# Optimization experiments

Hardware: AMD Instinct MI355X
Metric: run time of the kernel (lower is better)

## Reference

```python
import jax, jax.numpy as jnp
import numpy as np

N = 100000
IN_CH = 128
HID = 16
HEADS = 8
OUT_CH = 16
E = 1600000
NEG_SLOPE = 0.2


def glorot(key, shape, fan_in, fan_out):
    lim = jnp.sqrt(6.0 / (fan_in + fan_out)).astype(jnp.float32)
    return jax.random.uniform(key, shape, jnp.float32, -lim, lim)


def setup_inputs() -> dict:
    key = jax.random.key(0)
    ks = jax.random.split(key, 10)
    x = jax.random.normal(ks[0], (N, IN_CH), jnp.float32)
    edge_index = jax.random.randint(ks[1], (2, E), 0, N, jnp.int32)
    # layer 1: GATConv(IN_CH, HID, heads=8), concat=True
    W1 = glorot(ks[2], (IN_CH, HEADS * HID), IN_CH, HEADS * HID)
    att_src1 = glorot(ks[3], (HEADS, HID), HID, 1)
    att_dst1 = glorot(ks[4], (HEADS, HID), HID, 1)
    b1 = jnp.zeros((HEADS * HID,), jnp.float32)
    # layer 2: GATConv(HID*8, OUT_CH, heads=1)
    W2 = glorot(ks[5], (HEADS * HID, OUT_CH), HEADS * HID, OUT_CH)
    att_src2 = glorot(ks[6], (1, OUT_CH), OUT_CH, 1)
    att_dst2 = glorot(ks[7], (1, OUT_CH), OUT_CH, 1)
    b2 = jnp.zeros((OUT_CH,), jnp.float32)
    return {"x": x, "edge_index": edge_index, "W1": W1, "att_src1": att_src1,
            "att_dst1": att_dst1, "b1": b1, "W2": W2, "att_src2": att_src2,
            "att_dst2": att_dst2, "b2": b2}


def gat_layer(x, src, tgt, W, a_src, a_dst, bias, heads, ch, n):
    # h: [N, H, C]
    h = (x @ W).reshape(n, heads, ch)
    alpha_s = jnp.sum(h * a_src[None], axis=-1)  # [N, H]
    alpha_d = jnp.sum(h * a_dst[None], axis=-1)  # [N, H]
    # per-edge attention logit (message flows src -> tgt)
    e = jax.nn.leaky_relu(alpha_s[src] + alpha_d[tgt], NEG_SLOPE)  # [E, H]
    # segment softmax over target node neighborhoods (stable)
    m = jax.ops.segment_max(e, tgt, num_segments=n)  # [N, H]
    e = jnp.exp(e - m[tgt])
    denom = jax.ops.segment_sum(e, tgt, num_segments=n)
    alpha = e / (denom[tgt] + 1e-16)  # [E, H]
    # weighted scatter-add of source features
    out = jax.ops.segment_sum(h[src] * alpha[:, :, None], tgt, num_segments=n)
    return out.reshape(n, heads * ch) + bias


def reference(x, edge_index, W1, att_src1, att_dst1, b1, W2, att_src2, att_dst2, b2):
    n = x.shape[0]
    loops = jnp.arange(n, dtype=edge_index.dtype)
    src = jnp.concatenate([edge_index[0], loops])
    tgt = jnp.concatenate([edge_index[1], loops])
    h = gat_layer(x, src, tgt, W1, att_src1, att_dst1, b1, HEADS, HID, n)
    h = jax.nn.elu(h)
    out = gat_layer(h, src, tgt, W2, att_src2, att_dst2, b2, 1, OUT_CH, n)
    return out
```

## Files before the change

kernel.cpp:

```cpp
#include <hip/hip_runtime.h>
#include <hip/hip_fp16.h>
#include <math.h>

#define IN_CH 128
#define HEADS 8
#define HID 16
#define OUT_CH 16
#define NEG 0.2f
#define NPB 256
#define MAXBUCK 400
#define AST 136

__device__ __forceinline__ float lrelu(float x){ return x > 0.f ? x : NEG * x; }
__device__ __forceinline__ float elu_fast(float x){ return x > 0.f ? x : __expf(x) - 1.f; }

typedef _Float16 half8 __attribute__((ext_vector_type(8)));
typedef float    f32x4 __attribute__((ext_vector_type(4)));

__global__ __launch_bounds__(256) void k_bhist(const int* __restrict__ tgt, int E, int nbuck, int epb,
                                               int* __restrict__ bcnt){
    __shared__ int hist[MAXBUCK];
    int tid = threadIdx.x;
    for (int i = tid; i < nbuck; i += 256) hist[i] = 0;
    __syncthreads();
    int start = blockIdx.x * epb, end = min(start + epb, E);
    for (int e = start + tid; e < end; e += 256) atomicAdd(&hist[tgt[e] >> 8], 1);
    __syncthreads();
    for (int i = tid; i < nbuck; i += 256) if (hist[i]) atomicAdd(&bcnt[i], hist[i]);
}

__global__ void k_bscan(const int* __restrict__ bcnt, int nbuck, int E,
                        int* __restrict__ boffs, int* __restrict__ bcur){
    __shared__ int s[512];
    int t = threadIdx.x;
    int v = (t < nbuck) ? bcnt[t] : 0;
    int orig = v;
    s[t] = v; __syncthreads();
    for (int off = 1; off < 512; off <<= 1){
        int u = (t >= off) ? s[t - off] : 0;
        __syncthreads();
        v += u; s[t] = v; __syncthreads();
    }
    if (t < nbuck){ boffs[t] = v - orig; bcur[t] = v - orig; }
    if (t == 0) boffs[nbuck] = E;
}

__global__ __launch_bounds__(256) void k_bscatter(const int* __restrict__ ei, int E, int nbuck, int epb,
                                                  int* __restrict__ bcur, int2* __restrict__ ebuck){
    __shared__ int hist[MAXBUCK];
    __shared__ int base[MAXBUCK];
    int tid = threadIdx.x;
    for (int i = tid; i < nbuck; i += 256) hist[i] = 0;
    __syncthreads();
    int start = blockIdx.x * epb, end = min(start + epb, E);
    for (int e = start + tid; e < end; e += 256) atomicAdd(&hist[ei[E + e] >> 8], 1);
    __syncthreads();
    for (int i = tid; i < nbuck; i += 256){
        base[i] = hist[i] ? atomicAdd(&bcur[i], hist[i]) : 0;
        hist[i] = 0;
    }
    __syncthreads();
    for (int e = start + tid; e < end; e += 256){
        int s = ei[e], t = ei[E + e];
        int b = t >> 8;
        int r = atomicAdd(&hist[b], 1);
        ebuck[base[b] + r] = make_int2(s, t);
    }
}

__global__ __launch_bounds__(256) void k_csr(const int2* __restrict__ ebuck, const int* __restrict__ boffs,
                                             int N, int E,
                                             int* __restrict__ offs, int* __restrict__ esrc){
    __shared__ int cnt[256];
    __shared__ int sscan[256];
    __shared__ int wcur[256];
    int b = blockIdx.x;
    int tid = threadIdx.x;
    int n0 = b * 256;
    int nn = min(256, N - n0);
    cnt[tid] = (tid < nn) ? 1 : 0;
    __syncthreads();
    int e0 = boffs[b], e1 = boffs[b + 1];
    for (int e = e0 + tid; e < e1; e += 256) atomicAdd(&cnt[ebuck[e].y & 255], 1);
    __syncthreads();
    int v = cnt[tid], orig = v;
    sscan[tid] = v; __syncthreads();
    for (int off = 1; off < 256; off <<= 1){
        int u = (tid >= off) ? sscan[tid - off] : 0;
        __syncthreads();
        v += u; sscan[tid] = v; __syncthreads();
    }
    int excl = v - orig;
    int gbase = e0 + n0;
    if (tid < nn){
        offs[n0 + tid] = gbase + excl;
        esrc[gbase + excl] = n0 + tid;
    }
    wcur[tid] = excl + 1;
    __syncthreads();
    for (int e = e0 + tid; e < e1; e += 256){
        int2 p = ebuck[e];
        int r = atomicAdd(&wcur[p.y & 255], 1);
        esrc[gbase + r] = p.x;
    }
    if (b == 0 && tid == 0) offs[N] = E + N;
}

__global__ __launch_bounds__(256) void k_gemm1(const float* __restrict__ x, const float* __restrict__ W1,
                                               __half* __restrict__ h1, int N, int NT){
    __shared__ _Float16 sB[128*AST];
    __shared__ _Float16 sA[2][64*AST];
    int tid = threadIdx.x;
    for (int i = tid; i < 128*128; i += 256){
        int k = i >> 7, c = i & 127;
        sB[c*AST + k] = (_Float16)W1[i];
    }
    int wave = tid >> 6, lane = tid & 63;
    int m = lane & 15, quad = lane >> 4;
    int rbase = wave * 16;

    float4 vr[8];
    int tile = blockIdx.x;
    #pragma unroll
    for (int i = 0; i < 8; ++i){
        int q = i*256 + tid;
        int r = q >> 5, seg = q & 31;
        int row = tile*64 + r;
        vr[i] = make_float4(0.f,0.f,0.f,0.f);
        if (tile < NT && row < N) vr[i] = *(const float4*)(x + (size_t)row*128 + seg*4);
    }
    int b = 0;
    for (; tile < NT; tile += gridDim.x){
        #pragma unroll
        for (int i = 0; i < 8; ++i){
            int q = i*256 + tid;
            int r = q >> 5, seg = q & 31;
            _Float16* dst = &sA[b][r*AST + seg*4];
            dst[0]=(_Float16)vr[i].x; dst[1]=(_Float16)vr[i].y;
            dst[2]=(_Float16)vr[i].z; dst[3]=(_Float16)vr[i].w;
        }
        __syncthreads();
        int tn = tile + gridDim.x;
        #pragma unroll
        for (int i = 0; i < 8; ++i){
            int q = i*256 + tid;
            int r = q >> 5, seg = q & 31;
            int row = tn*64 + r;
            vr[i] = make_float4(0.f,0.f,0.f,0.f);
            if (tn < NT && row < N) vr[i] = *(const float4*)(x + (size_t)row*128 + seg*4);
        }
        f32x4 acc[8] = {};
        #pragma unroll
        for (int kc = 0; kc < 4; ++kc){
            int kb = kc*32 + quad*8;
            half8 a = *(half8*)(&sA[b][(rbase + m)*AST + kb]);
            #pragma unroll
            for (int t = 0; t < 8; ++t){
                half8 bb = *(half8*)(&sB[(t*16 + m)*AST + kb]);
                acc[t] = __builtin_amdgcn_mfma_f32_16x16x32_f16(a, bb, acc[t], 0, 0, 0);
            }
        }
        int row0 = tile*64;
        #pragma unroll
        for (int t = 0; t < 8; ++t){
            #pragma unroll
            for (int j = 0; j < 4; ++j){
                int r = row0 + rbase + quad*4 + j;
                if (r < N) h1[(size_t)r*128 + t*16 + m] = __float2half(acc[t][j]);
            }
        }
        b ^= 1;
    }
}

struct H8 { __half2 v[8]; };

__global__ void k_alpha1(const __half2* __restrict__ h1h, const float* __restrict__ asrc, const float* __restrict__ adst,
                         float2* __restrict__ asw, float* __restrict__ ad1,
                         unsigned char* __restrict__ h1q, int N){
    int idx = blockIdx.x*blockDim.x + threadIdx.x;
    if (idx >= N*HEADS) return;
    int h = idx & 7;
    int n = idx >> 3;
    H8 blk = *(const H8*)(h1h + (size_t)n*64 + h*8);
    const float2* sp = (const float2*)(asrc + h*16);
    const float2* dp = (const float2*)(adst + h*16);
    float fv[16];
    float ss = 0.f, dd = 0.f;
    #pragma unroll
    for (int j = 0; j < 8; ++j){
        float2 v = __half22float2(blk.v[j]);
        fv[2*j] = v.x; fv[2*j+1] = v.y;
        float2 a = sp[j], b = dp[j];
        ss += v.x*a.x + v.y*a.y;
        dd += v.x*b.x + v.y*b.y;
    }
    float mx = 1e-12f;
    #pragma unroll
    for (int k = 0; k < 16; ++k) mx = fmaxf(mx, fabsf(fv[k]));
    float rs = 127.f / mx;
    unsigned int w[4];
    #pragma unroll
    for (int d = 0; d < 4; ++d){
        unsigned int b0 = (unsigned int)((int)rintf(fv[4*d+0]*rs) + 128);
        unsigned int b1 = (unsigned int)((int)rintf(fv[4*d+1]*rs) + 128);
        unsigned int b2 = (unsigned int)((int)rintf(fv[4*d+2]*rs) + 128);
        unsigned int b3 = (unsigned int)((int)rintf(fv[4*d+3]*rs) + 128);
        w[d] = b0 | (b1 << 8) | (b2 << 16) | (b3 << 24);
    }
    asw[idx] = make_float2(ss, mx * (1.f/127.f));
    ad1[idx] = dd;
    *(uint4*)(h1q + (size_t)idx*16) = make_uint4(w[0], w[1], w[2], w[3]);
}

__global__ __launch_bounds__(256) void k_agg1(const unsigned char* __restrict__ h1q, const float2* __restrict__ asw,
                                              const float* __restrict__ ad1,
                                              const int* __restrict__ offs, const int* __restrict__ esrc,
                                              const float* __restrict__ b1, __half2* __restrict__ hl2h,
                                              int nbase, int nend){
    int wv = threadIdx.x >> 6;
    int l  = threadIdx.x & 63;
    int nsub = l >> 5;
    int slot = (l >> 3) & 3;
    int c    = l & 7;
    int n = nbase + blockIdx.x*8 + wv*2 + nsub;
    bool alive = (n < nend);
    float adc = 0.f;
    int e0 = 0, deg = 0;
    if (alive){
        adc = ad1[n*8 + c];
        e0 = offs[n];
        deg = offs[n+1] - e0;
    }
    int degmax = max(deg, __shfl_xor(deg, 32));

    float acc[16] = {};
    float den = 0.f;
    float dq  = 0.f;
    for (int i = 0; i < degmax; i += 8){
        int j0 = i + slot, j1 = i + 4 + slot;
        bool v0 = j0 < deg, v1 = j1 < deg;
        int iA = e0 + (v0 ? j0 : 0);
        int iB = e0 + (v1 ? j1 : 0);
        int s0 = esrc[iA], s1 = esrc[iB];
        float2 aw0 = asw[s0*8 + c];
        float2 aw1 = asw[s1*8 + c];
        uint4 q0 = *(const uint4*)(h1q + (size_t)s0*128 + c*16);
        uint4 q1 = *(const uint4*)(h1q + (size_t)s1*128 + c*16);
        float w0 = v0 ? __expf(lrelu(aw0.x + adc)) : 0.f;
        float w1 = v1 ? __expf(lrelu(aw1.x + adc)) : 0.f;
        float wq0 = w0 * aw0.y;
        float wq1 = w1 * aw1.y;
        den += w0 + w1;
        dq  += wq0 + wq1;
        const unsigned int* u0 = (const unsigned int*)&q0;
        const unsigned int* u1 = (const unsigned int*)&q1;
        #pragma unroll
        for (int d = 0; d < 4; ++d){
            unsigned int a = u0[d], b = u1[d];
            acc[4*d+0] += wq0 * (float)(a & 255u);
            acc[4*d+1] += wq0 * (float)((a >> 8) & 255u);
            acc[4*d+2] += wq0 * (float)((a >> 16) & 255u);
            acc[4*d+3] += wq0 * (float)(a >> 24);
            acc[4*d+0] += wq1 * (float)(b & 255u);
            acc[4*d+1] += wq1 * (float)((b >> 8) & 255u);
            acc[4*d+2] += wq1 * (float)((b >> 16) & 255u);
            acc[4*d+3] += wq1 * (float)(b >> 24);
        }
    }
    den += __shfl_xor(den, 8);  den += __shfl_xor(den, 16);
    dq  += __shfl_xor(dq, 8);   dq  += __shfl_xor(dq, 16);
    #pragma unroll
    for (int k = 0; k < 16; ++k){
        acc[k] += __shfl_xor(acc[k], 8);
        acc[k] += __shfl_xor(acc[k], 16);
    }
    if (!alive) return;
    float rd = 1.f / (den + 1e-16f);
    float bias128 = 128.f * dq;
    float sel0, sel1, sel2, sel3;
    {
        float a0 = (slot & 1) ? acc[4]  : acc[0];
        float b0 = (slot & 1) ? acc[12] : acc[8];
        sel0 = (slot & 2) ? b0 : a0;
        float a1 = (slot & 1) ? acc[5]  : acc[1];
        float b1v = (slot & 1) ? acc[13] : acc[9];
        sel1 = (slot & 2) ? b1v : a1;
        float a2 = (slot & 1) ? acc[6]  : acc[2];
        float b2v = (slot & 1) ? acc[14] : acc[10];
        sel2 = (slot & 2) ? b2v : a2;
        float a3 = (slot & 1) ? acc[7]  : acc[3];
        float b3v = (slot & 1) ? acc[15] : acc[11];
        sel3 = (slot & 2) ? b3v : a3;
    }
    float4 b4 = *(const float4*)(b1 + c*16 + slot*4);
    float v0 = elu_fast((sel0 - bias128)*rd + b4.x);
    float v1 = elu_fast((sel1 - bias128)*rd + b4.y);
    float v2 = elu_fast((sel2 - bias128)*rd + b4.z);
    float v3 = elu_fast((sel3 - bias128)*rd + b4.w);
    __half2 q0h = __floats2half2_rn(v0, v1);
    __half2 q1h = __floats2half2_rn(v2, v3);
    float2 ov;
    *(__half2*)&ov.x = q0h; *(__half2*)&ov.y = q1h;
    *(float2*)(hl2h + (size_t)n*64 + c*8 + slot*2) = ov;
}

#define FMA4(acc, a, b) { acc.x += (a)*(b).x; acc.y += (a)*(b).y; acc.z += (a)*(b).z; acc.w += (a)*(b).w; }

__global__ __launch_bounds__(256) void k_gemm2(const __half2* __restrict__ hl2h, const float* __restrict__ W2,
                                               const float* __restrict__ asrc2, const float* __restrict__ adst2,
                                               __half2* __restrict__ h2h, float* __restrict__ as2, float* __restrict__ ad2,
                                               int N){
    __shared__ float sX[64*132];
    __shared__ float sW2[128*16];
    int tid = threadIdx.x;
    for (int i = tid; i < 128*16; i += 256) sW2[i] = W2[i];
    int row0 = blockIdx.x * 64;
    #pragma unroll
    for (int i = 0; i < 4; ++i){
        int q = i*256 + tid;
        int r = q >> 4, seg = q & 15;
        float4 raw = make_float4(0.f,0.f,0.f,0.f);
        if (row0 + r < N) raw = ((const float4*)(hl2h + (size_t)(row0+r)*64))[seg];
        const __half2* hp = (const __half2*)&raw;
        float* dst = &sX[r*132 + seg*8];
        #pragma unroll
        for (int j = 0; j < 4; ++j){
            float2 f = __half22float2(hp[j]);
            dst[2*j] = f.x; dst[2*j+1] = f.y;
        }
    }
    __syncthreads();
    int nd = tid >> 2;
    int cq = tid & 3, c0 = cq*4;
    int n = row0 + nd;
    float4 acc = make_float4(0.f,0.f,0.f,0.f);
    #pragma unroll 4
    for (int k4 = 0; k4 < 32; ++k4){
        float4 a  = *(const float4*)(&sX[nd*132 + k4*4]);
        float4 w0 = *(const float4*)(&sW2[(k4*4+0)*16 + c0]);
        float4 w1 = *(const float4*)(&sW2[(k4*4+1)*16 + c0]);
        float4 w2 = *(const float4*)(&sW2[(k4*4+2)*16 + c0]);
        float4 w3 = *(const float4*)(&sW2[(k4*4+3)*16 + c0]);
        FMA4(acc, a.x, w0); FMA4(acc, a.y, w1); FMA4(acc, a.z, w2); FMA4(acc, a.w, w3);
    }
    float ps = acc.x*asrc2[c0] + acc.y*asrc2[c0+1] + acc.z*asrc2[c0+2] + acc.w*asrc2[c0+3];
    float pd = acc.x*adst2[c0] + acc.y*adst2[c0+1] + acc.z*adst2[c0+2] + acc.w*adst2[c0+3];
    ps += __shfl_xor(ps, 1); ps += __shfl_xor(ps, 2);
    pd += __shfl_xor(pd, 1); pd += __shfl_xor(pd, 2);
    if (n < N){
        __half2 p0 = __floats2half2_rn(acc.x, acc.y);
        __half2 p1 = __floats2half2_rn(acc.z, acc.w);
        float2 ov;
        *(__half2*)&ov.x = p0; *(__half2*)&ov.y = p1;
        *(float2*)(h2h + (size_t)n*8 + cq*2) = ov;
        if (cq == 0){ as2[n] = ps; ad2[n] = pd; }
    }
}

__global__ __launch_bounds__(256) void k_agg2(const __half2* __restrict__ h2h, const float* __restrict__ as2v,
                                              const float* __restrict__ ad2v,
                                              const int* __restrict__ offs, const int* __restrict__ esrc,
                                              const float* __restrict__ b2, float* __restrict__ out, int N){
    int n = blockIdx.x*4 + (threadIdx.x >> 6);
    if (n >= N) return;
    int l = threadIdx.x & 63;
    int e0 = offs[n], e1 = offs[n+1];
    float ad = ad2v[n];
    int eo = l >> 3, c2 = l & 7;
    float ax = 0.f, ay = 0.f, den = 0.f;
    for (int e = e0 + eo; e < e1; e += 8){
        int s = esrc[e];
        float w = __expf(lrelu(as2v[s] + ad));
        den += w;
        float2 f = __half22float2(h2h[(size_t)s*8 + c2]);
        ax += w * f.x; ay += w * f.y;
    }
    ax += __shfl_xor(ax, 8);  ay += __shfl_xor(ay, 8);  den += __shfl_xor(den, 8);
    ax += __shfl_xor(ax, 16); ay += __shfl_xor(ay, 16); den += __shfl_xor(den, 16);
    ax += __shfl_xor(ax, 32); ay += __shfl_xor(ay, 32); den += __shfl_xor(den, 32);
    if (eo == 0){
        float rd = 1.f / (den + 1e-16f);
        float2 bb = *(const float2*)(b2 + c2*2);
        float2 o = make_float2(ax*rd + bb.x, ay*rd + bb.y);
        *(float2*)(out + (size_t)n*16 + c2*2) = o;
    }
}

extern "C" void kernel_launch(void* const* d_in, const int* in_sizes, int n_in,
                              void* d_out, int out_size, void* d_ws, size_t ws_size,
                              hipStream_t stream){
    const float* x     = (const float*)d_in[0];
    const int*   ei    = (const int*)  d_in[1];
    const float* W1    = (const float*)d_in[2];
    const float* asrc1 = (const float*)d_in[3];
    const float* adst1 = (const float*)d_in[4];
    const float* b1    = (const float*)d_in[5];
    const float* W2    = (const float*)d_in[6];
    const float* asrc2 = (const float*)d_in[7];
    const float* adst2 = (const float*)d_in[8];
    const float* b2    = (const float*)d_in[9];
    float* out = (float*)d_out;

    const int N = in_sizes[0] / IN_CH;
    const int E = in_sizes[1] / 2;
    const int ETOT = E + N;
    const int NBUCK = (N + NPB - 1) / NPB;

    char* p = (char*)d_ws;
    auto alloc = [&](size_t bytes) -> char* {
        char* r = p; p += (bytes + 255) & ~(size_t)255; return r;
    };
    __half2* h1h  = (__half2*)alloc((size_t)N * 64 * 4);
    __half2* hl2h = (__half2*)alloc((size_t)N * 64 * 4);
    unsigned char* h1q = (unsigned char*)alloc((size_t)N * 128);
    float2* asw  = (float2*)alloc((size_t)N * 8 * 8);
    float* ad1   = (float*)alloc((size_t)N * 8 * 4);
    __half2* h2h = (__half2*)alloc((size_t)N * 8 * 4);
    float* as2   = (float*)alloc((size_t)N * 4);
    float* ad2   = (float*)alloc((size_t)N * 4);
    int*   bcnt  = (int*)  alloc((size_t)MAXBUCK * 4);
    int*   boffs = (int*)  alloc((size_t)(MAXBUCK + 1) * 4);
    int*   bcur  = (int*)  alloc((size_t)MAXBUCK * 4);
    int*   offs  = (int*)  alloc((size_t)(N + 1) * 4);
    int*   esrc  = (int*)  alloc((size_t)ETOT * 4);
    int2*  ebuck = (int2*)hl2h;

    (void)hipMemsetAsync(bcnt, 0, (size_t)NBUCK * 4, stream);

    const int GPART = 512;
    const int epb = (E + GPART - 1) / GPART;

    k_bhist   <<<GPART, 256, 0, stream>>>(ei + E, E, NBUCK, epb, bcnt);
    k_bscan   <<<1,     512, 0, stream>>>(bcnt, NBUCK, E, boffs, bcur);
    k_bscatter<<<GPART, 256, 0, stream>>>(ei, E, NBUCK, epb, bcur, ebuck);
    k_csr     <<<NBUCK, 256, 0, stream>>>(ebuck, boffs, N, E, offs, esrc);

    const int NT = (N + 63) / 64;
    const int G1 = NT < 512 ? NT : 512;
    k_gemm1  <<<G1, 256, 0, stream>>>(x, W1, (__half*)h1h, N, NT);
    k_alpha1 <<<(N * HEADS + 255) / 256, 256, 0, stream>>>(h1h, asrc1, adst1, asw, ad1, h1q, N);

    const int NH = ((N / 2) + 7) & ~7;
    k_agg1 <<<(NH + 7) / 8, 256, 0, stream>>>(h1q, asw, ad1, offs, esrc, b1, hl2h, 0, NH);
    k_agg1 <<<((N - NH) + 7) / 8, 256, 0, stream>>>(h1q, asw, ad1, offs, esrc, b1, hl2h, NH, N);

    k_gemm2  <<<(N + 63) / 64, 256, 0, stream>>>(hl2h, W2, asrc2, adst2, h2h, as2, ad2, N);
    k_agg2   <<<(N + 3) / 4, 256, 0, stream>>>(h2h, as2, ad2, offs, esrc, b2, out, N);
}
```

Measured before the change: 308.3 us.

## Replace two-level bucket sort CSR build with per-node atomic counting sort

The CSR construction no longer bucket-sorts edges by target block into an intermediate int2 buffer and then locally sorts each bucket. It now builds the CSR directly: global atomics give per-node degree counts, a two-level scan produces offsets, and a second pass of global atomics scatters each edge into its slot. This removes the intermediate buffer and its extra read/write pass, but trades shared-memory atomics for about two million contended global atomics and random writes into esrc. It also changes edge order within each segment to nondeterministic.

```diff
diff --git a/kernel.cpp b/kernel.cpp
--- a/kernel.cpp
+++ b/kernel.cpp
@@ -7,8 +7,7 @@
 #define HID 16
 #define OUT_CH 16
 #define NEG 0.2f
-#define NPB 256
-#define MAXBUCK 400
+#define MAXB 512
 #define AST 136
 
 __device__ __forceinline__ float lrelu(float x){ return x > 0.f ? x : NEG * x; }
@@ -17,23 +16,32 @@
 typedef _Float16 half8 __attribute__((ext_vector_type(8)));
 typedef float    f32x4 __attribute__((ext_vector_type(4)));
 
-__global__ __launch_bounds__(256) void k_bhist(const int* __restrict__ tgt, int E, int nbuck, int epb,
-                                               int* __restrict__ bcnt){
-    __shared__ int hist[MAXBUCK];
-    int tid = threadIdx.x;
-    for (int i = tid; i < nbuck; i += 256) hist[i] = 0;
-    __syncthreads();
-    int start = blockIdx.x * epb, end = min(start + epb, E);
-    for (int e = start + tid; e < end; e += 256) atomicAdd(&hist[tgt[e] >> 8], 1);
-    __syncthreads();
-    for (int i = tid; i < nbuck; i += 256) if (hist[i]) atomicAdd(&bcnt[i], hist[i]);
-}
-
-__global__ void k_bscan(const int* __restrict__ bcnt, int nbuck, int E,
-                        int* __restrict__ boffs, int* __restrict__ bcur){
+__global__ __launch_bounds__(256) void k_hist(const int* __restrict__ tgt, int E, int* __restrict__ cnt){
+    int e = blockIdx.x*256 + threadIdx.x;
+    if (e < E) atomicAdd(&cnt[tgt[e]], 1);
+}
+
+__global__ __launch_bounds__(256) void k_scanA(const int* __restrict__ cnt, int N,
+                                               int* __restrict__ offs, int* __restrict__ btot){
+    __shared__ int s[256];
+    int b = blockIdx.x, tid = threadIdx.x;
+    int i = b*256 + tid;
+    int v = (i < N) ? (cnt[i] + 1) : 0;
+    int orig = v;
+    s[tid] = v; __syncthreads();
+    for (int off = 1; off < 256; off <<= 1){
+        int u = (tid >= off) ? s[tid - off] : 0;
+        __syncthreads();
+        v += u; s[tid] = v; __syncthreads();
+    }
+    if (i < N) offs[i] = v - orig;
+    if (tid == 255) btot[b] = v;
+}
+
+__global__ void k_scanB(const int* __restrict__ btot, int nb, int* __restrict__ bbase){
     __shared__ int s[512];
     int t = threadIdx.x;
-    int v = (t < nbuck) ? bcnt[t] : 0;
+    int v = (t < nb) ? btot[t] : 0;
     int orig = v;
     s[t] = v; __syncthreads();
     for (int off = 1; off < 512; off <<= 1){
@@ -41,69 +49,29 @@
         __syncthreads();
         v += u; s[t] = v; __syncthreads();
     }
-    if (t < nbuck){ boffs[t] = v - orig; bcur[t] = v - orig; }
-    if (t == 0) boffs[nbuck] = E;
-}
-
-__global__ __launch_bounds__(256) void k_bscatter(const int* __restrict__ ei, int E, int nbuck, int epb,
-                                                  int* __restrict__ bcur, int2* __restrict__ ebuck){
-    __shared__ int hist[MAXBUCK];
-    __shared__ int base[MAXBUCK];
-    int tid = threadIdx.x;
-    for (int i = tid; i < nbuck; i += 256) hist[i] = 0;
-    __syncthreads();
-    int start = blockIdx.x * epb, end = min(start + epb, E);
-    for (int e = start + tid; e < end; e += 256) atomicAdd(&hist[ei[E + e] >> 8], 1);
-    __syncthreads();
-    for (int i = tid; i < nbuck; i += 256){
-        base[i] = hist[i] ? atomicAdd(&bcur[i], hist[i]) : 0;
-        hist[i] = 0;
-    }
-    __syncthreads();
-    for (int e = start + tid; e < end; e += 256){
+    if (t < nb) bbase[t] = v - orig;
+}
+
+__global__ __launch_bounds__(256) void k_finish(int* __restrict__ offs, const int* __restrict__ bbase,
+                                                int* __restrict__ cur, int* __restrict__ esrc, int N, int E){
+    int i = blockIdx.x*256 + threadIdx.x;
+    if (i < N){
+        int o = offs[i] + bbase[i >> 8];
+        offs[i] = o;
+        esrc[o] = i;
+        cur[i] = o + 1;
+    }
+    if (i == 0) offs[N] = E + N;
+}
+
+__global__ __launch_bounds__(256) void k_scatter(const int* __restrict__ ei, int E,
+                                                 int* __restrict__ cur, int* __restrict__ esrc){
+    int e = blockIdx.x*256 + threadIdx.x;
+    if (e < E){
         int s = ei[e], t = ei[E + e];
-        int b = t >> 8;
-        int r = atomicAdd(&hist[b], 1);
-        ebuck[base[b] + r] = make_int2(s, t);
-    }
-}
-
-__global__ __launch_bounds__(256) void k_csr(const int2* __restrict__ ebuck, const int* __restrict__ boffs,
-                                             int N, int E,
-                                             int* __restrict__ offs, int* __restrict__ esrc){
-    __shared__ int cnt[256];
-    __shared__ int sscan[256];
-    __shared__ int wcur[256];
-    int b = blockIdx.x;
-    int tid = threadIdx.x;
-    int n0 = b * 256;
-    int nn = min(256, N - n0);
-    cnt[tid] = (tid < nn) ? 1 : 0;
-    __syncthreads();
-    int e0 = boffs[b], e1 = boffs[b + 1];
-    for (int e = e0 + tid; e < e1; e += 256) atomicAdd(&cnt[ebuck[e].y & 255], 1);
-    __syncthreads();
-    int v = cnt[tid], orig = v;
-    sscan[tid] = v; __syncthreads();
-    for (int off = 1; off < 256; off <<= 1){
-        int u = (tid >= off) ? sscan[tid - off] : 0;
-        __syncthreads();
-        v += u; sscan[tid] = v; __syncthreads();
-    }
-    int excl = v - orig;
-    int gbase = e0 + n0;
-    if (tid < nn){
-        offs[n0 + tid] = gbase + excl;
-        esrc[gbase + excl] = n0 + tid;
-    }
-    wcur[tid] = excl + 1;
-    __syncthreads();
-    for (int e = e0 + tid; e < e1; e += 256){
-        int2 p = ebuck[e];
-        int r = atomicAdd(&wcur[p.y & 255], 1);
-        esrc[gbase + r] = p.x;
-    }
-    if (b == 0 && tid == 0) offs[N] = E + N;
+        int pos = atomicAdd(&cur[t], 1);
+        esrc[pos] = s;
+    }
 }
 
 __global__ __launch_bounds__(256) void k_gemm1(const float* __restrict__ x, const float* __restrict__ W1,
@@ -405,7 +373,7 @@
     const int N = in_sizes[0] / IN_CH;
     const int E = in_sizes[1] / 2;
     const int ETOT = E + N;
-    const int NBUCK = (N + NPB - 1) / NPB;
+    const int NB = (N + 255) / 256;
 
     char* p = (char*)d_ws;
     auto alloc = [&](size_t bytes) -> char* {
@@ -419,22 +387,20 @@
     __half2* h2h = (__half2*)alloc((size_t)N * 8 * 4);
     float* as2   = (float*)alloc((size_t)N * 4);
     float* ad2   = (float*)alloc((size_t)N * 4);
-    int*   bcnt  = (int*)  alloc((size_t)MAXBUCK * 4);
-    int*   boffs = (int*)  alloc((size_t)(MAXBUCK + 1) * 4);
-    int*   bcur  = (int*)  alloc((size_t)MAXBUCK * 4);
+    int*   cnt   = (int*)  alloc((size_t)N * 4);
+    int*   cur   = (int*)  alloc((size_t)N * 4);
+    int*   btot  = (int*)  alloc((size_t)MAXB * 4);
+    int*   bbase = (int*)  alloc((size_t)MAXB * 4);
     int*   offs  = (int*)  alloc((size_t)(N + 1) * 4);
     int*   esrc  = (int*)  alloc((size_t)ETOT * 4);
-    int2*  ebuck = (int2*)hl2h;
-
-    (void)hipMemsetAsync(bcnt, 0, (size_t)NBUCK * 4, stream);
-
-    const int GPART = 512;
-    const int epb = (E + GPART - 1) / GPART;
-
-    k_bhist   <<<GPART, 256, 0, stream>>>(ei + E, E, NBUCK, epb, bcnt);
-    k_bscan   <<<1,     512, 0, stream>>>(bcnt, NBUCK, E, boffs, bcur);
-    k_bscatter<<<GPART, 256, 0, stream>>>(ei, E, NBUCK, epb, bcur, ebuck);
-    k_csr     <<<NBUCK, 256, 0, stream>>>(ebuck, boffs, N, E, offs, esrc);
+
+    (void)hipMemsetAsync(cnt, 0, (size_t)N * 4, stream);
+
+    k_hist   <<<(E + 255) / 256, 256, 0, stream>>>(ei + E, E, cnt);
+    k_scanA  <<<NB, 256, 0, stream>>>(cnt, N, offs, btot);
+    k_scanB  <<<1, 512, 0, stream>>>(btot, NB, bbase);
+    k_finish <<<NB, 256, 0, stream>>>(offs, bbase, cur, esrc, N, E);
+    k_scatter<<<(E + 255) / 256, 256, 0, stream>>>(ei, E, cur, esrc);
 
     const int NT = (N + 63) / 64;
     const int G1 = NT < 512 ? NT : 512;
```

Result: slower. 442.3 us (+43.4%).

## Pack bucketed edges into 32-bit words, widen CSR blocks, pre-gather layer-2 source logits

Applied to the files above, without the earlier changes.

The bucket scatter now stores each edge as one 32-bit word, with the source index in the low 24 bits and the target's low byte in the high 8 bits, halving the intermediate edge buffer traffic. The CSR build kernel runs 512 threads per block to stream bucket edges faster. A new k_wprep kernel gathers as2[esrc[e]] into a contiguous per-edge array, so k_agg2 reads the source logit coalesced instead of doing a random gather. The extra kernel adds one more random-gather pass over all edges plus a write and read of a per-edge array, and the packing assumes node ids fit in 24 bits.

```diff
diff --git a/kernel.cpp b/kernel.cpp
--- a/kernel.cpp
+++ b/kernel.cpp
@@ -46,7 +46,7 @@
 }
 
 __global__ __launch_bounds__(256) void k_bscatter(const int* __restrict__ ei, int E, int nbuck, int epb,
-                                                  int* __restrict__ bcur, int2* __restrict__ ebuck){
+                                                  int* __restrict__ bcur, int* __restrict__ ebuck){
     __shared__ int hist[MAXBUCK];
     __shared__ int base[MAXBUCK];
     int tid = threadIdx.x;
@@ -64,11 +64,11 @@
         int s = ei[e], t = ei[E + e];
         int b = t >> 8;
         int r = atomicAdd(&hist[b], 1);
-        ebuck[base[b] + r] = make_int2(s, t);
-    }
-}
-
-__global__ __launch_bounds__(256) void k_csr(const int2* __restrict__ ebuck, const int* __restrict__ boffs,
+        ebuck[base[b] + r] = s | ((t & 255) << 24);
+    }
+}
+
+__global__ __launch_bounds__(512) void k_csr(const int* __restrict__ ebuck, const int* __restrict__ boffs,
                                              int N, int E,
                                              int* __restrict__ offs, int* __restrict__ esrc){
     __shared__ int cnt[256];
@@ -78,30 +78,34 @@
     int tid = threadIdx.x;
     int n0 = b * 256;
     int nn = min(256, N - n0);
-    cnt[tid] = (tid < nn) ? 1 : 0;
+    if (tid < 256) cnt[tid] = (tid < nn) ? 1 : 0;
     __syncthreads();
     int e0 = boffs[b], e1 = boffs[b + 1];
-    for (int e = e0 + tid; e < e1; e += 256) atomicAdd(&cnt[ebuck[e].y & 255], 1);
-    __syncthreads();
-    int v = cnt[tid], orig = v;
-    sscan[tid] = v; __syncthreads();
+    for (int e = e0 + tid; e < e1; e += 512) atomicAdd(&cnt[((unsigned)ebuck[e]) >> 24], 1);
+    __syncthreads();
+    int v = 0, orig = 0;
+    if (tid < 256){ v = cnt[tid]; orig = v; sscan[tid] = v; }
+    __syncthreads();
     for (int off = 1; off < 256; off <<= 1){
-        int u = (tid >= off) ? sscan[tid - off] : 0;
+        int u = (tid < 256 && tid >= off) ? sscan[tid - off] : 0;
         __syncthreads();
-        v += u; sscan[tid] = v; __syncthreads();
-    }
-    int excl = v - orig;
+        if (tid < 256){ v += u; sscan[tid] = v; }
+        __syncthreads();
+    }
     int gbase = e0 + n0;
-    if (tid < nn){
-        offs[n0 + tid] = gbase + excl;
-        esrc[gbase + excl] = n0 + tid;
-    }
-    wcur[tid] = excl + 1;
-    __syncthreads();
-    for (int e = e0 + tid; e < e1; e += 256){
-        int2 p = ebuck[e];
-        int r = atomicAdd(&wcur[p.y & 255], 1);
-        esrc[gbase + r] = p.x;
+    if (tid < 256){
+        int excl = v - orig;
+        if (tid < nn){
+            offs[n0 + tid] = gbase + excl;
+            esrc[gbase + excl] = n0 + tid;
+        }
+        wcur[tid] = excl + 1;
+    }
+    __syncthreads();
+    for (int e = e0 + tid; e < e1; e += 512){
+        int w = ebuck[e];
+        int r = atomicAdd(&wcur[((unsigned)w) >> 24], 1);
+        esrc[gbase + r] = w & 0xFFFFFF;
     }
     if (b == 0 && tid == 0) offs[N] = E + N;
 }
@@ -358,7 +362,13 @@
     }
 }
 
-__global__ __launch_bounds__(256) void k_agg2(const __half2* __restrict__ h2h, const float* __restrict__ as2v,
+__global__ __launch_bounds__(256) void k_wprep(const int* __restrict__ esrc, const float* __restrict__ as2,
+                                               float* __restrict__ ws, int M){
+    int i = blockIdx.x*256 + threadIdx.x;
+    if (i < M) ws[i] = as2[esrc[i]];
+}
+
+__global__ __launch_bounds__(256) void k_agg2(const __half2* __restrict__ h2h, const float* __restrict__ ws,
                                               const float* __restrict__ ad2v,
                                               const int* __restrict__ offs, const int* __restrict__ esrc,
                                               const float* __restrict__ b2, float* __restrict__ out, int N){
@@ -371,7 +381,7 @@
     float ax = 0.f, ay = 0.f, den = 0.f;
     for (int e = e0 + eo; e < e1; e += 8){
         int s = esrc[e];
-        float w = __expf(lrelu(as2v[s] + ad));
+        float w = __expf(lrelu(ws[e] + ad));
         den += w;
         float2 f = __half22float2(h2h[(size_t)s*8 + c2]);
         ax += w * f.x; ay += w * f.y;
@@ -424,7 +434,8 @@
     int*   bcur  = (int*)  alloc((size_t)MAXBUCK * 4);
     int*   offs  = (int*)  alloc((size_t)(N + 1) * 4);
     int*   esrc  = (int*)  alloc((size_t)ETOT * 4);
-    int2*  ebuck = (int2*)hl2h;
+    float* wsb   = (float*)alloc((size_t)ETOT * 4);
+    int*   ebuck = (int*)hl2h;
 
     (void)hipMemsetAsync(bcnt, 0, (size_t)NBUCK * 4, stream);
 
@@ -434,7 +445,7 @@
     k_bhist   <<<GPART, 256, 0, stream>>>(ei + E, E, NBUCK, epb, bcnt);
     k_bscan   <<<1,     512, 0, stream>>>(bcnt, NBUCK, E, boffs, bcur);
     k_bscatter<<<GPART, 256, 0, stream>>>(ei, E, NBUCK, epb, bcur, ebuck);
-    k_csr     <<<NBUCK, 256, 0, stream>>>(ebuck, boffs, N, E, offs, esrc);
+    k_csr     <<<NBUCK, 512, 0, stream>>>(ebuck, boffs, N, E, offs, esrc);
 
     const int NT = (N + 63) / 64;
     const int G1 = NT < 512 ? NT : 512;
@@ -446,5 +457,6 @@
     k_agg1 <<<((N - NH) + 7) / 8, 256, 0, stream>>>(h1q, asw, ad1, offs, esrc, b1, hl2h, NH, N);
 
     k_gemm2  <<<(N + 63) / 64, 256, 0, stream>>>(hl2h, W2, asrc2, adst2, h2h, as2, ad2, N);
-    k_agg2   <<<(N + 3) / 4, 256, 0, stream>>>(h2h, as2, ad2, offs, esrc, b2, out, N);
-}
+    k_wprep  <<<(ETOT + 255) / 256, 256, 0, stream>>>(esrc, as2, wsb, ETOT);
+    k_agg2   <<<(N + 3) / 4, 256, 0, stream>>>(h2h, wsb, ad2, offs, esrc, b2, out, N);
+}
```

New measurement: 319.7 us. 3.7% more time.
